# Performance work log

Measured on AMD Instinct MI355X. Metric: run time of the kernel, lower is better.

The kernel has to match this reference:

```python
import jax, jax.numpy as jnp
import numpy as np

B, S, E, D, H = 32, 4096, 512, 512, 512


def setup_inputs() -> dict:
    key = jax.random.key(0)
    ks = jax.random.split(key, 7)
    scale = 1.0 / np.sqrt(H)
    return {
        "encoder_hiddens": jax.random.normal(ks[0], (B, S, E), dtype=jnp.float32),
        "decoder_hidden": jax.random.normal(ks[1], (B, D), dtype=jnp.float32),
        "W_enc": jax.random.uniform(ks[2], (H, E), jnp.float32, -scale, scale),
        "b_enc": jax.random.uniform(ks[3], (H,), jnp.float32, -scale, scale),
        "W_dec": jax.random.uniform(ks[4], (H, D), jnp.float32, -scale, scale),
        "b_dec": jax.random.uniform(ks[5], (H,), jnp.float32, -scale, scale),
        "v": jax.random.uniform(ks[6], (H,), jnp.float32, -scale, scale),
    }


def reference(encoder_hiddens, decoder_hidden, W_enc, b_enc, W_dec, b_dec, v):
    # Projections (the two small GEMMs of the original per-timestep loop, batched)
    enc_hs = jnp.einsum("bse,he->bsh", encoder_hiddens, W_enc) + b_enc  # [B,S,H]
    dec_h = decoder_hidden @ W_dec.T + b_dec                            # [B,H]

    # Ragged-length detection: the torch loop breaks at the first all-zero
    # projected encoder row; positions at/after that are excluded (cumulative AND).
    nonzero = jnp.any(enc_hs != 0, axis=-1)                             # [B,S]
    valid = jnp.cumprod(nonzero.astype(jnp.int32), axis=1).astype(bool)

    # Additive (Bahdanau) scores: v . tanh(enc_hs + dec_h)
    scores = jnp.einsum("h,bsh->bs", v, jnp.tanh(enc_hs + dec_h[:, None, :]))
    scores = jnp.where(valid, scores, -jnp.inf)
    attn = jax.nn.softmax(scores, axis=1)                               # [B,S]
    attn = jnp.where(valid, attn, 0.0)

    # Weighted sum of encoder states -> context vector [B,1,E]
    return jnp.sum(encoder_hiddens * attn[..., None], axis=1, keepdims=True)
```

## Files before the change

### kernel.cpp

```cpp
#include <hip/hip_runtime.h>
#include <hip/hip_bf16.h>

#define BATCH 32
#define SEQ   4096
#define EDIM  512
#define HDIM  512

typedef unsigned short u16;
typedef unsigned int   u32;

typedef __bf16 bf16x8 __attribute__((ext_vector_type(8)));
typedef float  f32x4  __attribute__((ext_vector_type(4)));

__device__ __forceinline__ u16 bf_rne(float x) {
    u32 u = __float_as_uint(x);
    u32 r = (u + 0x7fffu + ((u >> 16) & 1u)) >> 16;
    return (u16)r;
}
__device__ __forceinline__ u32 pack2(u16 lo, u16 hi) {
    return (u32)lo | ((u32)hi << 16);
}
__device__ __forceinline__ float tanh_fast(float x) {
    float e = __builtin_amdgcn_exp2f(x * 2.88539008177793f);
    return 1.0f - 2.0f * __builtin_amdgcn_rcpf(e + 1.0f);
}

__global__ void pack_w(const float* __restrict__ W, uint4* __restrict__ out) {
    int id   = blockIdx.x * 256 + threadIdx.x;
    int nsub = id >> 10;
    int rem  = id & 1023;
    int kc   = rem >> 6;
    int lane = rem & 63;
    int row  = nsub * 16 + (lane & 15);
    int col  = kc * 32 + (lane >> 4) * 8;
    const float* src = W + row * EDIM + col;
    uint4 o;
    o.x = pack2(bf_rne(src[0]), bf_rne(src[1]));
    o.y = pack2(bf_rne(src[2]), bf_rne(src[3]));
    o.z = pack2(bf_rne(src[4]), bf_rne(src[5]));
    o.w = pack2(bf_rne(src[6]), bf_rne(src[7]));
    out[id] = o;
}

__global__ void dec_proj(const float* __restrict__ dec, const float* __restrict__ Wd,
                         const float* __restrict__ b_enc, const float* __restrict__ b_dec,
                         float* __restrict__ out) {
    int wave = threadIdx.x >> 6, lane = threadIdx.x & 63;
    int p = blockIdx.x * 4 + wave;
    int b = p >> 9, h = p & 511;
    const float4* wr = reinterpret_cast<const float4*>(Wd)  + h * 128;
    const float4* dr = reinterpret_cast<const float4*>(dec) + b * 128;
    float4 w0 = wr[lane * 2], w1 = wr[lane * 2 + 1];
    float4 d0 = dr[lane * 2], d1 = dr[lane * 2 + 1];
    float s = w0.x * d0.x + w0.y * d0.y + w0.z * d0.z + w0.w * d0.w
            + w1.x * d1.x + w1.y * d1.y + w1.z * d1.z + w1.w * d1.w;
#pragma unroll
    for (int m = 1; m < 64; m <<= 1) s += __shfl_xor(s, m, 64);
    if (lane == 0) out[p] = s + b_dec[h] + b_enc[h];
}

__global__ __launch_bounds__(256, 2) void score_kernel(
    const float* __restrict__ X, const uint4* __restrict__ Wp,
    const float* __restrict__ bias, const float* __restrict__ v,
    float* __restrict__ scores)
{
    __shared__ alignas(16) u16 Abuf[2][64 * 40];
    __shared__ float sred[4][64];

    const int tid  = threadIdx.x;
    const int wave = tid >> 6, lane = tid & 63;
    const int quad = lane >> 4, l15 = lane & 15;
    const int blk  = blockIdx.x;
    const long row0 = (long)blk * 64;
    const int b = blk >> 6;
    const float4* X4 = reinterpret_cast<const float4*>(X + row0 * EDIM);

    float hb[8], hv[8];
#pragma unroll
    for (int jj = 0; jj < 8; jj++) {
        int h = wave * 128 + jj * 16 + l15;
        hb[jj] = bias[b * HDIM + h];
        hv[jj] = v[h];
    }

    f32x4 acc[4][8] = {};
    float s_acc[16];
#pragma unroll
    for (int i = 0; i < 16; i++) s_acc[i] = 0.f;

    const int r0 = tid >> 3;
    const int c0 = tid & 7;
    const int r1 = r0 + 32;

    float4 pa = X4[r0 * 128 + c0];
    float4 pb = X4[r1 * 128 + c0];
    {
        uint2 s0 = make_uint2(pack2(bf_rne(pa.x), bf_rne(pa.y)),
                              pack2(bf_rne(pa.z), bf_rne(pa.w)));
        uint2 s1 = make_uint2(pack2(bf_rne(pb.x), bf_rne(pb.y)),
                              pack2(bf_rne(pb.z), bf_rne(pb.w)));
        *reinterpret_cast<uint2*>(&Abuf[0][r0 * 40 + c0 * 4]) = s0;
        *reinterpret_cast<uint2*>(&Abuf[0][r1 * 40 + c0 * 4]) = s1;
    }
    pa = X4[r0 * 128 + 8 + c0];
    pb = X4[r1 * 128 + 8 + c0];
    __syncthreads();

#pragma unroll
    for (int ch = 0; ch < 16; ch++) {
        const int c = ch & 1;
        if (ch < 15) {
            uint2 s0 = make_uint2(pack2(bf_rne(pa.x), bf_rne(pa.y)),
                                  pack2(bf_rne(pa.z), bf_rne(pa.w)));
            uint2 s1 = make_uint2(pack2(bf_rne(pb.x), bf_rne(pb.y)),
                                  pack2(bf_rne(pb.z), bf_rne(pb.w)));
            *reinterpret_cast<uint2*>(&Abuf[c ^ 1][r0 * 40 + c0 * 4]) = s0;
            *reinterpret_cast<uint2*>(&Abuf[c ^ 1][r1 * 40 + c0 * 4]) = s1;
        }
        if (ch < 14) {
            int k4 = (ch + 2) * 8;
            pa = X4[r0 * 128 + k4 + c0];
            pb = X4[r1 * 128 + k4 + c0];
        }
        uint4 braw[8];
#pragma unroll
        for (int jj = 0; jj < 8; jj++)
            braw[jj] = Wp[((wave * 8 + jj) * 16 + ch) * 64 + lane];
        bf16x8 af[4];
#pragma unroll
        for (int i = 0; i < 4; i++)
            af[i] = *reinterpret_cast<const bf16x8*>(&Abuf[c][(i * 16 + l15) * 40 + quad * 8]);
#pragma unroll
        for (int jj = 0; jj < 8; jj++) {
            bf16x8 bfr = __builtin_bit_cast(bf16x8, braw[jj]);
#pragma unroll
            for (int i = 0; i < 4; i++)
                acc[i][jj] = __builtin_amdgcn_mfma_f32_16x16x32_bf16(
                    af[i], bfr, acc[i][jj], 0, 0, 0);
        }
        __syncthreads();
    }

#pragma unroll
    for (int i = 0; i < 4; i++)
#pragma unroll
        for (int jj = 0; jj < 8; jj++)
#pragma unroll
            for (int r = 0; r < 4; r++) {
                float val = acc[i][jj][r] + hb[jj];
                s_acc[i * 4 + r] += hv[jj] * tanh_fast(val);
            }

#pragma unroll
    for (int m = 1; m < 16; m <<= 1)
#pragma unroll
        for (int x = 0; x < 16; x++)
            s_acc[x] += __shfl_xor(s_acc[x], m, 16);

    if (l15 == 0) {
#pragma unroll
        for (int x = 0; x < 16; x++) {
            int i = x >> 2, r = x & 3;
            sred[wave][i * 16 + quad * 4 + r] = s_acc[x];
        }
    }
    __syncthreads();
    if (tid < 64) {
        scores[row0 + tid] = sred[0][tid] + sred[1][tid] + sred[2][tid] + sred[3][tid];
    }
}

__global__ void softmax_k(const float* __restrict__ scores, float* __restrict__ attn) {
    __shared__ float redmax[4], redsum[4];
    int b = blockIdx.x, t = threadIdx.x;
    int wave = t >> 6, lane = t & 63;
    const float* sb = scores + b * SEQ;
    float vals[16];
    float mx = -1e30f;
#pragma unroll
    for (int i = 0; i < 16; i++) { vals[i] = sb[i * 256 + t]; mx = fmaxf(mx, vals[i]); }
#pragma unroll
    for (int m = 1; m < 64; m <<= 1) mx = fmaxf(mx, __shfl_xor(mx, m, 64));
    if (lane == 0) redmax[wave] = mx;
    __syncthreads();
    mx = fmaxf(fmaxf(redmax[0], redmax[1]), fmaxf(redmax[2], redmax[3]));
    float s = 0.f;
#pragma unroll
    for (int i = 0; i < 16; i++) {
        float e = __builtin_amdgcn_exp2f((vals[i] - mx) * 1.44269504088896f);
        vals[i] = e; s += e;
    }
#pragma unroll
    for (int m = 1; m < 64; m <<= 1) s += __shfl_xor(s, m, 64);
    if (lane == 0) redsum[wave] = s;
    __syncthreads();
    s = redsum[0] + redsum[1] + redsum[2] + redsum[3];
    float inv = 1.0f / s;
    float* ab = attn + b * SEQ;
#pragma unroll
    for (int i = 0; i < 16; i++) ab[i * 256 + t] = vals[i] * inv;
}

__global__ __launch_bounds__(256) void context_k(const float* __restrict__ X,
                                                 const float* __restrict__ attn,
                                                 float* __restrict__ out) {
    __shared__ float aw[64];
    int blk = blockIdx.x;
    int b = blk >> 6, s0 = (blk & 63) << 6;
    int t = threadIdx.x;
    if (t < 64) aw[t] = attn[b * SEQ + s0 + t];
    __syncthreads();
    const float2* Xp = reinterpret_cast<const float2*>(X) + ((long)(b * SEQ + s0)) * 256 + t;
    float ax0 = 0.f, ay0 = 0.f, ax1 = 0.f, ay1 = 0.f;
#pragma unroll 4
    for (int s = 0; s < 64; s += 8) {
        float2 x[8];
#pragma unroll
        for (int k = 0; k < 8; k++) x[k] = Xp[(long)(s + k) * 256];
#pragma unroll
        for (int k = 0; k < 8; k += 2) {
            float w0 = aw[s + k], w1 = aw[s + k + 1];
            ax0 = fmaf(w0, x[k].x,     ax0);
            ay0 = fmaf(w0, x[k].y,     ay0);
            ax1 = fmaf(w1, x[k + 1].x, ax1);
            ay1 = fmaf(w1, x[k + 1].y, ay1);
        }
    }
    atomicAdd(&out[b * EDIM + t * 2],     ax0 + ax1);
    atomicAdd(&out[b * EDIM + t * 2 + 1], ay0 + ay1);
}

extern "C" void kernel_launch(void* const* d_in, const int* in_sizes, int n_in,
                              void* d_out, int out_size, void* d_ws, size_t ws_size,
                              hipStream_t stream) {
    const float* X      = (const float*)d_in[0];
    const float* dec    = (const float*)d_in[1];
    const float* W_enc  = (const float*)d_in[2];
    const float* b_enc  = (const float*)d_in[3];
    const float* W_dec  = (const float*)d_in[4];
    const float* b_dec  = (const float*)d_in[5];
    const float* v      = (const float*)d_in[6];
    float* out = (float*)d_out;

    char* ws = (char*)d_ws;
    uint4* wpack    = (uint4*)ws;
    float* dec_bias = (float*)(ws + (512 << 10));
    float* scores   = (float*)(ws + (512 << 10) + (64 << 10));
    float* attn     = (float*)(ws + (1024 << 10) + (64 << 10));

    hipMemsetAsync(d_out, 0, 32 * EDIM * sizeof(float), stream);

    pack_w   <<<128,  256, 0, stream>>>(W_enc, wpack);
    dec_proj <<<4096, 256, 0, stream>>>(dec, W_dec, b_enc, b_dec, dec_bias);
    score_kernel<<<2048, 256, 0, stream>>>(X, wpack, dec_bias, v, scores);
    softmax_k<<<32,   256, 0, stream>>>(scores, attn);
    context_k<<<2048, 256, 0, stream>>>(X, attn, out);
}
```

Measured before the change: 478.5 us.

## Merge prep kernels and enlarge score tile to 128 rows with 512 threads

Folds the weight packing, decoder projection and output zeroing into one launch, removing two kernel launches and a memset. The score kernel now processes 128 rows per block with 8 waves: two M-halves share each packed weight fragment, and each double-buffered phase covers K=64 instead of K=32. This halves the weight-fragment traffic per row and halves the number of block barriers. In exchange the block uses more LDS and registers, launches fewer blocks, and issues deeper per-phase loads, so occupancy may drop.

```diff
diff --git a/kernel.cpp b/kernel.cpp
--- a/kernel.cpp
+++ b/kernel.cpp
@@ -25,131 +25,149 @@
     return 1.0f - 2.0f * __builtin_amdgcn_rcpf(e + 1.0f);
 }
 
-__global__ void pack_w(const float* __restrict__ W, uint4* __restrict__ out) {
-    int id   = blockIdx.x * 256 + threadIdx.x;
-    int nsub = id >> 10;
-    int rem  = id & 1023;
-    int kc   = rem >> 6;
-    int lane = rem & 63;
-    int row  = nsub * 16 + (lane & 15);
-    int col  = kc * 32 + (lane >> 4) * 8;
-    const float* src = W + row * EDIM + col;
-    uint4 o;
-    o.x = pack2(bf_rne(src[0]), bf_rne(src[1]));
-    o.y = pack2(bf_rne(src[2]), bf_rne(src[3]));
-    o.z = pack2(bf_rne(src[4]), bf_rne(src[5]));
-    o.w = pack2(bf_rne(src[6]), bf_rne(src[7]));
-    out[id] = o;
-}
-
-__global__ void dec_proj(const float* __restrict__ dec, const float* __restrict__ Wd,
-                         const float* __restrict__ b_enc, const float* __restrict__ b_dec,
-                         float* __restrict__ out) {
-    int wave = threadIdx.x >> 6, lane = threadIdx.x & 63;
-    int p = blockIdx.x * 4 + wave;
-    int b = p >> 9, h = p & 511;
-    const float4* wr = reinterpret_cast<const float4*>(Wd)  + h * 128;
-    const float4* dr = reinterpret_cast<const float4*>(dec) + b * 128;
-    float4 w0 = wr[lane * 2], w1 = wr[lane * 2 + 1];
-    float4 d0 = dr[lane * 2], d1 = dr[lane * 2 + 1];
-    float s = w0.x * d0.x + w0.y * d0.y + w0.z * d0.z + w0.w * d0.w
-            + w1.x * d1.x + w1.y * d1.y + w1.z * d1.z + w1.w * d1.w;
-#pragma unroll
-    for (int m = 1; m < 64; m <<= 1) s += __shfl_xor(s, m, 64);
-    if (lane == 0) out[p] = s + b_dec[h] + b_enc[h];
-}
-
-__global__ __launch_bounds__(256, 2) void score_kernel(
+__global__ void prep_kernel(const float* __restrict__ W_enc, uint4* __restrict__ wpack,
+                            const float* __restrict__ dec, const float* __restrict__ Wd,
+                            const float* __restrict__ b_enc, const float* __restrict__ b_dec,
+                            float* __restrict__ dec_bias, float* __restrict__ out) {
+    int bid = blockIdx.x;
+    int t = threadIdx.x;
+    if (bid < 4096) {
+        int wave = t >> 6, lane = t & 63;
+        int p = bid * 4 + wave;
+        int b = p >> 9, h = p & 511;
+        const float4* wr = reinterpret_cast<const float4*>(Wd)  + h * 128;
+        const float4* dr = reinterpret_cast<const float4*>(dec) + b * 128;
+        float4 w0 = wr[lane * 2], w1 = wr[lane * 2 + 1];
+        float4 d0 = dr[lane * 2], d1 = dr[lane * 2 + 1];
+        float s = w0.x * d0.x + w0.y * d0.y + w0.z * d0.z + w0.w * d0.w
+                + w1.x * d1.x + w1.y * d1.y + w1.z * d1.z + w1.w * d1.w;
+#pragma unroll
+        for (int m = 1; m < 64; m <<= 1) s += __shfl_xor(s, m, 64);
+        if (lane == 0) dec_bias[p] = s + b_dec[h] + b_enc[h];
+    } else if (bid < 4224) {
+        int id   = (bid - 4096) * 256 + t;
+        int nsub = id >> 10;
+        int rem  = id & 1023;
+        int kc   = rem >> 6;
+        int lane = rem & 63;
+        int row  = nsub * 16 + (lane & 15);
+        int col  = kc * 32 + (lane >> 4) * 8;
+        const float* src = W_enc + row * EDIM + col;
+        uint4 o;
+        o.x = pack2(bf_rne(src[0]), bf_rne(src[1]));
+        o.y = pack2(bf_rne(src[2]), bf_rne(src[3]));
+        o.z = pack2(bf_rne(src[4]), bf_rne(src[5]));
+        o.w = pack2(bf_rne(src[6]), bf_rne(src[7]));
+        wpack[id] = o;
+    } else {
+        float4 z = make_float4(0.f, 0.f, 0.f, 0.f);
+        float4* o4 = reinterpret_cast<float4*>(out);
+#pragma unroll
+        for (int i = 0; i < 16; i++) o4[i * 256 + t] = z;
+    }
+}
+
+__global__ __launch_bounds__(512, 2) void score_kernel(
     const float* __restrict__ X, const uint4* __restrict__ Wp,
     const float* __restrict__ bias, const float* __restrict__ v,
     float* __restrict__ scores)
 {
-    __shared__ alignas(16) u16 Abuf[2][64 * 40];
-    __shared__ float sred[4][64];
+    __shared__ alignas(16) u16 Abuf[2][128 * 72];
+    __shared__ float sred[8][64];
 
     const int tid  = threadIdx.x;
     const int wave = tid >> 6, lane = tid & 63;
     const int quad = lane >> 4, l15 = lane & 15;
-    const int blk  = blockIdx.x;
-    const long row0 = (long)blk * 64;
-    const int b = blk >> 6;
+    const int mh = wave >> 2;
+    const int ns = wave & 3;
+    const int blk = blockIdx.x;
+    const long row0 = (long)blk * 128;
+    const int b = blk >> 5;
     const float4* X4 = reinterpret_cast<const float4*>(X + row0 * EDIM);
 
+    f32x4 acc[4][8] = {};
+
+    const int r = tid >> 2;
+    const int s = tid & 3;
+
+    {
+        float4 p0[4];
+#pragma unroll
+        for (int i = 0; i < 4; i++) p0[i] = X4[r * 128 + s * 4 + i];
+#pragma unroll
+        for (int i = 0; i < 4; i++) {
+            uint2 w = make_uint2(pack2(bf_rne(p0[i].x), bf_rne(p0[i].y)),
+                                 pack2(bf_rne(p0[i].z), bf_rne(p0[i].w)));
+            *reinterpret_cast<uint2*>(&Abuf[0][r * 72 + (s * 4 + i) * 4]) = w;
+        }
+    }
+    __syncthreads();
+
+#pragma unroll 2
+    for (int ph = 0; ph < 8; ph++) {
+        const int cur = ph & 1;
+        const u16* Ab = Abuf[cur];
+
+        uint4 braw[16];
+#pragma unroll
+        for (int ks = 0; ks < 2; ks++)
+#pragma unroll
+            for (int jj = 0; jj < 8; jj++)
+                braw[ks * 8 + jj] = Wp[((ns * 8 + jj) * 16 + ph * 2 + ks) * 64 + lane];
+
+        float4 pf[4];
+        if (ph < 7) {
+#pragma unroll
+            for (int i = 0; i < 4; i++)
+                pf[i] = X4[r * 128 + (ph + 1) * 16 + s * 4 + i];
+        }
+
+#pragma unroll
+        for (int ks = 0; ks < 2; ks++) {
+            bf16x8 af[4];
+#pragma unroll
+            for (int i = 0; i < 4; i++)
+                af[i] = *reinterpret_cast<const bf16x8*>(
+                    &Ab[(mh * 64 + i * 16 + l15) * 72 + ks * 32 + quad * 8]);
+#pragma unroll
+            for (int jj = 0; jj < 8; jj++) {
+                bf16x8 bfr = __builtin_bit_cast(bf16x8, braw[ks * 8 + jj]);
+#pragma unroll
+                for (int i = 0; i < 4; i++)
+                    acc[i][jj] = __builtin_amdgcn_mfma_f32_16x16x32_bf16(
+                        af[i], bfr, acc[i][jj], 0, 0, 0);
+            }
+        }
+
+        if (ph < 7) {
+#pragma unroll
+            for (int i = 0; i < 4; i++) {
+                uint2 w = make_uint2(pack2(bf_rne(pf[i].x), bf_rne(pf[i].y)),
+                                     pack2(bf_rne(pf[i].z), bf_rne(pf[i].w)));
+                *reinterpret_cast<uint2*>(&Abuf[cur ^ 1][r * 72 + (s * 4 + i) * 4]) = w;
+            }
+        }
+        __syncthreads();
+    }
+
     float hb[8], hv[8];
 #pragma unroll
     for (int jj = 0; jj < 8; jj++) {
-        int h = wave * 128 + jj * 16 + l15;
+        int h = ns * 128 + jj * 16 + l15;
         hb[jj] = bias[b * HDIM + h];
         hv[jj] = v[h];
     }
 
-    f32x4 acc[4][8] = {};
     float s_acc[16];
 #pragma unroll
-    for (int i = 0; i < 16; i++) s_acc[i] = 0.f;
-
-    const int r0 = tid >> 3;
-    const int c0 = tid & 7;
-    const int r1 = r0 + 32;
-
-    float4 pa = X4[r0 * 128 + c0];
-    float4 pb = X4[r1 * 128 + c0];
-    {
-        uint2 s0 = make_uint2(pack2(bf_rne(pa.x), bf_rne(pa.y)),
-                              pack2(bf_rne(pa.z), bf_rne(pa.w)));
-        uint2 s1 = make_uint2(pack2(bf_rne(pb.x), bf_rne(pb.y)),
-                              pack2(bf_rne(pb.z), bf_rne(pb.w)));
-        *reinterpret_cast<uint2*>(&Abuf[0][r0 * 40 + c0 * 4]) = s0;
-        *reinterpret_cast<uint2*>(&Abuf[0][r1 * 40 + c0 * 4]) = s1;
-    }
-    pa = X4[r0 * 128 + 8 + c0];
-    pb = X4[r1 * 128 + 8 + c0];
-    __syncthreads();
-
-#pragma unroll
-    for (int ch = 0; ch < 16; ch++) {
-        const int c = ch & 1;
-        if (ch < 15) {
-            uint2 s0 = make_uint2(pack2(bf_rne(pa.x), bf_rne(pa.y)),
-                                  pack2(bf_rne(pa.z), bf_rne(pa.w)));
-            uint2 s1 = make_uint2(pack2(bf_rne(pb.x), bf_rne(pb.y)),
-                                  pack2(bf_rne(pb.z), bf_rne(pb.w)));
-            *reinterpret_cast<uint2*>(&Abuf[c ^ 1][r0 * 40 + c0 * 4]) = s0;
-            *reinterpret_cast<uint2*>(&Abuf[c ^ 1][r1 * 40 + c0 * 4]) = s1;
-        }
-        if (ch < 14) {
-            int k4 = (ch + 2) * 8;
-            pa = X4[r0 * 128 + k4 + c0];
-            pb = X4[r1 * 128 + k4 + c0];
-        }
-        uint4 braw[8];
+    for (int x = 0; x < 16; x++) s_acc[x] = 0.f;
+#pragma unroll
+    for (int i = 0; i < 4; i++)
 #pragma unroll
         for (int jj = 0; jj < 8; jj++)
-            braw[jj] = Wp[((wave * 8 + jj) * 16 + ch) * 64 + lane];
-        bf16x8 af[4];
-#pragma unroll
-        for (int i = 0; i < 4; i++)
-            af[i] = *reinterpret_cast<const bf16x8*>(&Abuf[c][(i * 16 + l15) * 40 + quad * 8]);
-#pragma unroll
-        for (int jj = 0; jj < 8; jj++) {
-            bf16x8 bfr = __builtin_bit_cast(bf16x8, braw[jj]);
-#pragma unroll
-            for (int i = 0; i < 4; i++)
-                acc[i][jj] = __builtin_amdgcn_mfma_f32_16x16x32_bf16(
-                    af[i], bfr, acc[i][jj], 0, 0, 0);
-        }
-        __syncthreads();
-    }
-
-#pragma unroll
-    for (int i = 0; i < 4; i++)
-#pragma unroll
-        for (int jj = 0; jj < 8; jj++)
-#pragma unroll
-            for (int r = 0; r < 4; r++) {
-                float val = acc[i][jj][r] + hb[jj];
-                s_acc[i * 4 + r] += hv[jj] * tanh_fast(val);
-            }
+#pragma unroll
+            for (int rr = 0; rr < 4; rr++)
+                s_acc[i * 4 + rr] += hv[jj] * tanh_fast(acc[i][jj][rr] + hb[jj]);
 
 #pragma unroll
     for (int m = 1; m < 16; m <<= 1)
@@ -160,13 +178,15 @@
     if (l15 == 0) {
 #pragma unroll
         for (int x = 0; x < 16; x++) {
-            int i = x >> 2, r = x & 3;
-            sred[wave][i * 16 + quad * 4 + r] = s_acc[x];
-        }
-    }
-    __syncthreads();
-    if (tid < 64) {
-        scores[row0 + tid] = sred[0][tid] + sred[1][tid] + sred[2][tid] + sred[3][tid];
+            int i = x >> 2, rr = x & 3;
+            sred[wave][i * 16 + quad * 4 + rr] = s_acc[x];
+        }
+    }
+    __syncthreads();
+    if (tid < 128) {
+        int mhh = tid >> 6, m = tid & 63;
+        scores[row0 + tid] = sred[mhh * 4 + 0][m] + sred[mhh * 4 + 1][m]
+                           + sred[mhh * 4 + 2][m] + sred[mhh * 4 + 3][m];
     }
 }
 
@@ -248,11 +268,9 @@
     float* scores   = (float*)(ws + (512 << 10) + (64 << 10));
     float* attn     = (float*)(ws + (1024 << 10) + (64 << 10));
 
-    hipMemsetAsync(d_out, 0, 32 * EDIM * sizeof(float), stream);
-
-    pack_w   <<<128,  256, 0, stream>>>(W_enc, wpack);
-    dec_proj <<<4096, 256, 0, stream>>>(dec, W_dec, b_enc, b_dec, dec_bias);
-    score_kernel<<<2048, 256, 0, stream>>>(X, wpack, dec_bias, v, scores);
-    softmax_k<<<32,   256, 0, stream>>>(scores, attn);
-    context_k<<<2048, 256, 0, stream>>>(X, attn, out);
-}
+    prep_kernel <<<4225, 256, 0, stream>>>(W_enc, wpack, dec, W_dec, b_enc, b_dec,
+                                           dec_bias, out);
+    score_kernel<<<1024, 512, 0, stream>>>(X, wpack, dec_bias, v, scores);
+    softmax_k   <<<32,   256, 0, stream>>>(scores, attn);
+    context_k   <<<2048, 256, 0, stream>>>(X, attn, out);
+}
```

After: 547.0 us. 14.3% more time.

## Fuse score, softmax and context into one flash-style kernel with partial combine

Applied to the files above, without the earlier changes.

Merges the score GEMM, softmax and weighted-context sum into one kernel. Each 64-row block computes local max and sum-exp, then reuses its X tile (likely still in L2) to build a partial context vector, and a small combine kernel rescales and sums the partials. The two weight-prep kernels become one launch, and the memset and atomics are removed. The goal is to avoid re-reading the full 256MB X from HBM in a separate pass and to cut launches. In exchange the workspace traffic for partials grows. The fused kernel now gives each thread a wider 16-byte LDS store layout, and its main loop is no longer unrolled.

```diff
diff --git a/kernel.cpp b/kernel.cpp
--- a/kernel.cpp
+++ b/kernel.cpp
@@ -5,6 +5,8 @@
 #define SEQ   4096
 #define EDIM  512
 #define HDIM  512
+#define NCHUNK 64
+#define NBLK  (BATCH * NCHUNK)
 
 typedef unsigned short u16;
 typedef unsigned int   u32;
@@ -25,55 +27,117 @@
     return 1.0f - 2.0f * __builtin_amdgcn_rcpf(e + 1.0f);
 }
 
-__global__ void pack_w(const float* __restrict__ W, uint4* __restrict__ out) {
-    int id   = blockIdx.x * 256 + threadIdx.x;
-    int nsub = id >> 10;
-    int rem  = id & 1023;
-    int kc   = rem >> 6;
-    int lane = rem & 63;
-    int row  = nsub * 16 + (lane & 15);
-    int col  = kc * 32 + (lane >> 4) * 8;
-    const float* src = W + row * EDIM + col;
-    uint4 o;
-    o.x = pack2(bf_rne(src[0]), bf_rne(src[1]));
-    o.y = pack2(bf_rne(src[2]), bf_rne(src[3]));
-    o.z = pack2(bf_rne(src[4]), bf_rne(src[5]));
-    o.w = pack2(bf_rne(src[6]), bf_rne(src[7]));
-    out[id] = o;
-}
-
-__global__ void dec_proj(const float* __restrict__ dec, const float* __restrict__ Wd,
-                         const float* __restrict__ b_enc, const float* __restrict__ b_dec,
-                         float* __restrict__ out) {
-    int wave = threadIdx.x >> 6, lane = threadIdx.x & 63;
-    int p = blockIdx.x * 4 + wave;
-    int b = p >> 9, h = p & 511;
-    const float4* wr = reinterpret_cast<const float4*>(Wd)  + h * 128;
-    const float4* dr = reinterpret_cast<const float4*>(dec) + b * 128;
-    float4 w0 = wr[lane * 2], w1 = wr[lane * 2 + 1];
-    float4 d0 = dr[lane * 2], d1 = dr[lane * 2 + 1];
-    float s = w0.x * d0.x + w0.y * d0.y + w0.z * d0.z + w0.w * d0.w
-            + w1.x * d1.x + w1.y * d1.y + w1.z * d1.z + w1.w * d1.w;
-#pragma unroll
-    for (int m = 1; m < 64; m <<= 1) s += __shfl_xor(s, m, 64);
-    if (lane == 0) out[p] = s + b_dec[h] + b_enc[h];
-}
-
-__global__ __launch_bounds__(256, 2) void score_kernel(
+__global__ void prep_kernel(const float* __restrict__ W_enc, uint4* __restrict__ wpack,
+                            const float* __restrict__ dec, const float* __restrict__ Wd,
+                            const float* __restrict__ b_enc, const float* __restrict__ b_dec,
+                            float* __restrict__ dec_bias) {
+    int bid = blockIdx.x;
+    int t = threadIdx.x;
+    if (bid < 4096) {
+        int wave = t >> 6, lane = t & 63;
+        int p = bid * 4 + wave;
+        int b = p >> 9, h = p & 511;
+        const float4* wr = reinterpret_cast<const float4*>(Wd)  + h * 128;
+        const float4* dr = reinterpret_cast<const float4*>(dec) + b * 128;
+        float4 w0 = wr[lane * 2], w1 = wr[lane * 2 + 1];
+        float4 d0 = dr[lane * 2], d1 = dr[lane * 2 + 1];
+        float s = w0.x * d0.x + w0.y * d0.y + w0.z * d0.z + w0.w * d0.w
+                + w1.x * d1.x + w1.y * d1.y + w1.z * d1.z + w1.w * d1.w;
+#pragma unroll
+        for (int m = 1; m < 64; m <<= 1) s += __shfl_xor(s, m, 64);
+        if (lane == 0) dec_bias[p] = s + b_dec[h] + b_enc[h];
+    } else {
+        int id   = (bid - 4096) * 256 + t;
+        int nsub = id >> 10;
+        int rem  = id & 1023;
+        int kc   = rem >> 6;
+        int lane = rem & 63;
+        int row  = nsub * 16 + (lane & 15);
+        int col  = kc * 32 + (lane >> 4) * 8;
+        const float* src = W_enc + row * EDIM + col;
+        uint4 o;
+        o.x = pack2(bf_rne(src[0]), bf_rne(src[1]));
+        o.y = pack2(bf_rne(src[2]), bf_rne(src[3]));
+        o.z = pack2(bf_rne(src[4]), bf_rne(src[5]));
+        o.w = pack2(bf_rne(src[6]), bf_rne(src[7]));
+        wpack[id] = o;
+    }
+}
+
+__global__ __launch_bounds__(256, 2) void fused_kernel(
     const float* __restrict__ X, const uint4* __restrict__ Wp,
     const float* __restrict__ bias, const float* __restrict__ v,
-    float* __restrict__ scores)
+    float* __restrict__ cpart, float* __restrict__ mpart, float* __restrict__ lpart)
 {
-    __shared__ alignas(16) u16 Abuf[2][64 * 40];
+    __shared__ alignas(16) u16 Abuf[2][64 * 72];
     __shared__ float sred[4][64];
+    __shared__ float pbuf[64];
 
     const int tid  = threadIdx.x;
     const int wave = tid >> 6, lane = tid & 63;
     const int quad = lane >> 4, l15 = lane & 15;
     const int blk  = blockIdx.x;
+    const int b    = blk >> 6;
     const long row0 = (long)blk * 64;
-    const int b = blk >> 6;
     const float4* X4 = reinterpret_cast<const float4*>(X + row0 * EDIM);
+
+    f32x4 acc[4][8] = {};
+
+    const int r  = tid >> 2;
+    const int c8 = tid & 3;
+
+    float4 pA = X4[r * 128 + c8 * 2];
+    float4 pB = X4[r * 128 + c8 * 2 + 1];
+    {
+        uint4 w;
+        w.x = pack2(bf_rne(pA.x), bf_rne(pA.y));
+        w.y = pack2(bf_rne(pA.z), bf_rne(pA.w));
+        w.z = pack2(bf_rne(pB.x), bf_rne(pB.y));
+        w.w = pack2(bf_rne(pB.z), bf_rne(pB.w));
+        *reinterpret_cast<uint4*>(&Abuf[0][r * 72 + c8 * 8]) = w;
+    }
+    pA = X4[r * 128 + 8 + c8 * 2];
+    pB = X4[r * 128 + 8 + c8 * 2 + 1];
+    __syncthreads();
+
+    for (int ch = 0; ch < 16; ch++) {
+        const u16* Ab = Abuf[ch & 1];
+
+        uint4 braw[8];
+#pragma unroll
+        for (int jj = 0; jj < 8; jj++)
+            braw[jj] = Wp[((wave * 8 + jj) * 16 + ch) * 64 + lane];
+
+        float4 nA, nB;
+        if (ch < 14) {
+            nA = X4[r * 128 + (ch + 2) * 8 + c8 * 2];
+            nB = X4[r * 128 + (ch + 2) * 8 + c8 * 2 + 1];
+        }
+
+        bf16x8 af[4];
+#pragma unroll
+        for (int i = 0; i < 4; i++)
+            af[i] = *reinterpret_cast<const bf16x8*>(&Ab[(i * 16 + l15) * 72 + quad * 8]);
+#pragma unroll
+        for (int jj = 0; jj < 8; jj++) {
+            bf16x8 bfr = __builtin_bit_cast(bf16x8, braw[jj]);
+#pragma unroll
+            for (int i = 0; i < 4; i++)
+                acc[i][jj] = __builtin_amdgcn_mfma_f32_16x16x32_bf16(
+                    af[i], bfr, acc[i][jj], 0, 0, 0);
+        }
+
+        if (ch < 15) {
+            uint4 w;
+            w.x = pack2(bf_rne(pA.x), bf_rne(pA.y));
+            w.y = pack2(bf_rne(pA.z), bf_rne(pA.w));
+            w.z = pack2(bf_rne(pB.x), bf_rne(pB.y));
+            w.w = pack2(bf_rne(pB.z), bf_rne(pB.w));
+            *reinterpret_cast<uint4*>(&Abuf[(ch & 1) ^ 1][r * 72 + c8 * 8]) = w;
+        }
+        __syncthreads();
+        if (ch < 14) { pA = nA; pB = nB; }
+    }
 
     float hb[8], hv[8];
 #pragma unroll
@@ -82,74 +146,16 @@
         hb[jj] = bias[b * HDIM + h];
         hv[jj] = v[h];
     }
-
-    f32x4 acc[4][8] = {};
     float s_acc[16];
 #pragma unroll
-    for (int i = 0; i < 16; i++) s_acc[i] = 0.f;
-
-    const int r0 = tid >> 3;
-    const int c0 = tid & 7;
-    const int r1 = r0 + 32;
-
-    float4 pa = X4[r0 * 128 + c0];
-    float4 pb = X4[r1 * 128 + c0];
-    {
-        uint2 s0 = make_uint2(pack2(bf_rne(pa.x), bf_rne(pa.y)),
-                              pack2(bf_rne(pa.z), bf_rne(pa.w)));
-        uint2 s1 = make_uint2(pack2(bf_rne(pb.x), bf_rne(pb.y)),
-                              pack2(bf_rne(pb.z), bf_rne(pb.w)));
-        *reinterpret_cast<uint2*>(&Abuf[0][r0 * 40 + c0 * 4]) = s0;
-        *reinterpret_cast<uint2*>(&Abuf[0][r1 * 40 + c0 * 4]) = s1;
-    }
-    pa = X4[r0 * 128 + 8 + c0];
-    pb = X4[r1 * 128 + 8 + c0];
-    __syncthreads();
-
-#pragma unroll
-    for (int ch = 0; ch < 16; ch++) {
-        const int c = ch & 1;
-        if (ch < 15) {
-            uint2 s0 = make_uint2(pack2(bf_rne(pa.x), bf_rne(pa.y)),
-                                  pack2(bf_rne(pa.z), bf_rne(pa.w)));
-            uint2 s1 = make_uint2(pack2(bf_rne(pb.x), bf_rne(pb.y)),
-                                  pack2(bf_rne(pb.z), bf_rne(pb.w)));
-            *reinterpret_cast<uint2*>(&Abuf[c ^ 1][r0 * 40 + c0 * 4]) = s0;
-            *reinterpret_cast<uint2*>(&Abuf[c ^ 1][r1 * 40 + c0 * 4]) = s1;
-        }
-        if (ch < 14) {
-            int k4 = (ch + 2) * 8;
-            pa = X4[r0 * 128 + k4 + c0];
-            pb = X4[r1 * 128 + k4 + c0];
-        }
-        uint4 braw[8];
+    for (int x = 0; x < 16; x++) s_acc[x] = 0.f;
+#pragma unroll
+    for (int i = 0; i < 4; i++)
 #pragma unroll
         for (int jj = 0; jj < 8; jj++)
-            braw[jj] = Wp[((wave * 8 + jj) * 16 + ch) * 64 + lane];
-        bf16x8 af[4];
-#pragma unroll
-        for (int i = 0; i < 4; i++)
-            af[i] = *reinterpret_cast<const bf16x8*>(&Abuf[c][(i * 16 + l15) * 40 + quad * 8]);
-#pragma unroll
-        for (int jj = 0; jj < 8; jj++) {
-            bf16x8 bfr = __builtin_bit_cast(bf16x8, braw[jj]);
-#pragma unroll
-            for (int i = 0; i < 4; i++)
-                acc[i][jj] = __builtin_amdgcn_mfma_f32_16x16x32_bf16(
-                    af[i], bfr, acc[i][jj], 0, 0, 0);
-        }
-        __syncthreads();
-    }
-
-#pragma unroll
-    for (int i = 0; i < 4; i++)
-#pragma unroll
-        for (int jj = 0; jj < 8; jj++)
-#pragma unroll
-            for (int r = 0; r < 4; r++) {
-                float val = acc[i][jj][r] + hb[jj];
-                s_acc[i * 4 + r] += hv[jj] * tanh_fast(val);
-            }
+#pragma unroll
+            for (int rr = 0; rr < 4; rr++)
+                s_acc[i * 4 + rr] += hv[jj] * tanh_fast(acc[i][jj][rr] + hb[jj]);
 
 #pragma unroll
     for (int m = 1; m < 16; m <<= 1)
@@ -160,74 +166,83 @@
     if (l15 == 0) {
 #pragma unroll
         for (int x = 0; x < 16; x++) {
-            int i = x >> 2, r = x & 3;
-            sred[wave][i * 16 + quad * 4 + r] = s_acc[x];
-        }
-    }
-    __syncthreads();
+            int i = x >> 2, rr = x & 3;
+            sred[wave][i * 16 + quad * 4 + rr] = s_acc[x];
+        }
+    }
+    __syncthreads();
+
     if (tid < 64) {
-        scores[row0 + tid] = sred[0][tid] + sred[1][tid] + sred[2][tid] + sred[3][tid];
-    }
-}
-
-__global__ void softmax_k(const float* __restrict__ scores, float* __restrict__ attn) {
-    __shared__ float redmax[4], redsum[4];
-    int b = blockIdx.x, t = threadIdx.x;
-    int wave = t >> 6, lane = t & 63;
-    const float* sb = scores + b * SEQ;
-    float vals[16];
-    float mx = -1e30f;
-#pragma unroll
-    for (int i = 0; i < 16; i++) { vals[i] = sb[i * 256 + t]; mx = fmaxf(mx, vals[i]); }
-#pragma unroll
-    for (int m = 1; m < 64; m <<= 1) mx = fmaxf(mx, __shfl_xor(mx, m, 64));
-    if (lane == 0) redmax[wave] = mx;
-    __syncthreads();
-    mx = fmaxf(fmaxf(redmax[0], redmax[1]), fmaxf(redmax[2], redmax[3]));
-    float s = 0.f;
-#pragma unroll
-    for (int i = 0; i < 16; i++) {
-        float e = __builtin_amdgcn_exp2f((vals[i] - mx) * 1.44269504088896f);
-        vals[i] = e; s += e;
-    }
-#pragma unroll
-    for (int m = 1; m < 64; m <<= 1) s += __shfl_xor(s, m, 64);
-    if (lane == 0) redsum[wave] = s;
-    __syncthreads();
-    s = redsum[0] + redsum[1] + redsum[2] + redsum[3];
-    float inv = 1.0f / s;
-    float* ab = attn + b * SEQ;
-#pragma unroll
-    for (int i = 0; i < 16; i++) ab[i * 256 + t] = vals[i] * inv;
-}
-
-__global__ __launch_bounds__(256) void context_k(const float* __restrict__ X,
-                                                 const float* __restrict__ attn,
-                                                 float* __restrict__ out) {
-    __shared__ float aw[64];
-    int blk = blockIdx.x;
-    int b = blk >> 6, s0 = (blk & 63) << 6;
-    int t = threadIdx.x;
-    if (t < 64) aw[t] = attn[b * SEQ + s0 + t];
-    __syncthreads();
-    const float2* Xp = reinterpret_cast<const float2*>(X) + ((long)(b * SEQ + s0)) * 256 + t;
+        float sc = sred[0][tid] + sred[1][tid] + sred[2][tid] + sred[3][tid];
+        float mx = sc;
+#pragma unroll
+        for (int m = 1; m < 64; m <<= 1) mx = fmaxf(mx, __shfl_xor(mx, m, 64));
+        float p = __builtin_amdgcn_exp2f((sc - mx) * 1.44269504088896f);
+        float l = p;
+#pragma unroll
+        for (int m = 1; m < 64; m <<= 1) l += __shfl_xor(l, m, 64);
+        pbuf[tid] = p;
+        if (tid == 0) { mpart[blk] = mx; lpart[blk] = l; }
+    }
+    __syncthreads();
+
+    const float2* Xp = reinterpret_cast<const float2*>(X + row0 * EDIM) + tid;
     float ax0 = 0.f, ay0 = 0.f, ax1 = 0.f, ay1 = 0.f;
-#pragma unroll 4
+#pragma unroll 2
     for (int s = 0; s < 64; s += 8) {
         float2 x[8];
 #pragma unroll
-        for (int k = 0; k < 8; k++) x[k] = Xp[(long)(s + k) * 256];
+        for (int k = 0; k < 8; k++) x[k] = Xp[(s + k) * 256];
 #pragma unroll
         for (int k = 0; k < 8; k += 2) {
-            float w0 = aw[s + k], w1 = aw[s + k + 1];
+            float w0 = pbuf[s + k], w1 = pbuf[s + k + 1];
             ax0 = fmaf(w0, x[k].x,     ax0);
             ay0 = fmaf(w0, x[k].y,     ay0);
             ax1 = fmaf(w1, x[k + 1].x, ax1);
             ay1 = fmaf(w1, x[k + 1].y, ay1);
         }
     }
-    atomicAdd(&out[b * EDIM + t * 2],     ax0 + ax1);
-    atomicAdd(&out[b * EDIM + t * 2 + 1], ay0 + ay1);
+    reinterpret_cast<float2*>(cpart)[blk * 256 + tid] =
+        make_float2(ax0 + ax1, ay0 + ay1);
+}
+
+__global__ __launch_bounds__(256) void combine_k(const float* __restrict__ cpart,
+                                                 const float* __restrict__ mpart,
+                                                 const float* __restrict__ lpart,
+                                                 float* __restrict__ out) {
+    __shared__ float wbuf[64];
+    __shared__ float linv_s;
+    int b = blockIdx.x, t = threadIdx.x;
+    if (t < 64) {
+        float m = mpart[b * 64 + t];
+        float M = m;
+#pragma unroll
+        for (int k = 1; k < 64; k <<= 1) M = fmaxf(M, __shfl_xor(M, k, 64));
+        float w = __builtin_amdgcn_exp2f((m - M) * 1.44269504088896f);
+        float lw = lpart[b * 64 + t] * w;
+        float L = lw;
+#pragma unroll
+        for (int k = 1; k < 64; k <<= 1) L += __shfl_xor(L, k, 64);
+        wbuf[t] = w;
+        if (t == 0) linv_s = 1.0f / L;
+    }
+    __syncthreads();
+    const float2* cp = reinterpret_cast<const float2*>(cpart) + (long)b * 64 * 256 + t;
+    float ax = 0.f, ay = 0.f;
+#pragma unroll 2
+    for (int i = 0; i < 64; i += 8) {
+        float2 x[8];
+#pragma unroll
+        for (int k = 0; k < 8; k++) x[k] = cp[(i + k) * 256];
+#pragma unroll
+        for (int k = 0; k < 8; k++) {
+            float w = wbuf[i + k];
+            ax = fmaf(w, x[k].x, ax);
+            ay = fmaf(w, x[k].y, ay);
+        }
+    }
+    float inv = linv_s;
+    reinterpret_cast<float2*>(out)[b * 256 + t] = make_float2(ax * inv, ay * inv);
 }
 
 extern "C" void kernel_launch(void* const* d_in, const int* in_sizes, int n_in,
@@ -245,14 +260,12 @@
     char* ws = (char*)d_ws;
     uint4* wpack    = (uint4*)ws;
     float* dec_bias = (float*)(ws + (512 << 10));
-    float* scores   = (float*)(ws + (512 << 10) + (64 << 10));
-    float* attn     = (float*)(ws + (1024 << 10) + (64 << 10));
-
-    hipMemsetAsync(d_out, 0, 32 * EDIM * sizeof(float), stream);
-
-    pack_w   <<<128,  256, 0, stream>>>(W_enc, wpack);
-    dec_proj <<<4096, 256, 0, stream>>>(dec, W_dec, b_enc, b_dec, dec_bias);
-    score_kernel<<<2048, 256, 0, stream>>>(X, wpack, dec_bias, v, scores);
-    softmax_k<<<32,   256, 0, stream>>>(scores, attn);
-    context_k<<<2048, 256, 0, stream>>>(X, attn, out);
-}
+    float* cpart    = (float*)(ws + (576 << 10));
+    float* mpart    = (float*)(ws + (576 << 10) + (4096 << 10));
+    float* lpart    = (float*)(ws + (576 << 10) + (4104 << 10));
+
+    prep_kernel  <<<4224, 256, 0, stream>>>(W_enc, wpack, dec, W_dec, b_enc, b_dec,
+                                            dec_bias);
+    fused_kernel <<<NBLK, 256, 0, stream>>>(X, wpack, dec_bias, v, cpart, mpart, lpart);
+    combine_k    <<<BATCH, 256, 0, stream>>>(cpart, mpart, lpart, out);
+}
```

Result: faster. 447.5 us (-6.5%).
